# Optimization experiments

Measured on AMD Instinct MI355X. Metric: run time of the kernel, lower is better.

## Reference

```python
import jax, jax.numpy as jnp
import numpy as np

V, NB, NJ, NP, NK = 6890, 10, 24, 207, 19
PARENTS = np.array([-1, 0, 0, 0, 1, 2, 3, 4, 5, 6, 7, 8, 9, 9, 9, 12, 13, 14, 16, 17, 18, 19, 20, 21])


def setup_inputs():
    key = jax.random.key(0)
    ks = jax.random.split(key, 9)
    B = 1024
    beta = jax.random.normal(ks[0], (B, NB), jnp.float32)
    theta = jax.random.normal(ks[1], (B, NJ * 3), jnp.float32) * 0.3  # axis-angle per joint
    trans = jax.random.normal(ks[2], (B, 3), jnp.float32)
    v_template = jax.random.normal(ks[3], (V, 3), jnp.float32)
    shapedirs = jax.random.normal(ks[4], (NB, V * 3), jnp.float32) * 0.03
    Jr = jax.random.uniform(ks[5], (V, NJ), jnp.float32)
    J_regressor = Jr / jnp.sum(Jr, axis=0, keepdims=True)
    posedirs = jax.random.normal(ks[6], (NP, V * 3), jnp.float32) * 0.01
    jr = jax.random.uniform(ks[7], (V, NK), jnp.float32)
    joint_regressor = jr / jnp.sum(jr, axis=0, keepdims=True)
    w = jax.random.uniform(ks[8], (V, NJ), jnp.float32)
    weights = w / jnp.sum(w, axis=1, keepdims=True)  # LBS weights, rows sum to 1
    return dict(beta=beta, theta=theta, trans=trans, v_template=v_template,
                shapedirs=shapedirs, J_regressor=J_regressor, posedirs=posedirs,
                joint_regressor=joint_regressor, weights=weights)


def batch_rodrigues(theta):
    # theta: (N,3) axis-angle -> (N,3,3) rotation matrices via quaternions (HMR-style)
    angle = jnp.linalg.norm(theta + 1e-8, axis=1, keepdims=True)
    half = angle * 0.5
    v = (theta / angle) * jnp.sin(half)
    quat = jnp.concatenate([jnp.cos(half), v], axis=1)
    quat = quat / jnp.linalg.norm(quat, axis=1, keepdims=True)
    w, x, y, z = quat[:, 0], quat[:, 1], quat[:, 2], quat[:, 3]
    rot = jnp.stack([
        1 - 2 * (y * y + z * z), 2 * (x * y - w * z), 2 * (x * z + w * y),
        2 * (x * y + w * z), 1 - 2 * (x * x + z * z), 2 * (y * z - w * x),
        2 * (x * z - w * y), 2 * (y * z + w * x), 1 - 2 * (x * x + y * y)], axis=1)
    return rot.reshape(-1, 3, 3)


def batch_global_rigid_transformation(Rs, J):
    # Rs: (B,24,3,3), J: (B,24,3); rotate_base=True
    B = Rs.shape[0]
    rot_x = jnp.array([[1., 0., 0.], [0., -1., 0.], [0., 0., -1.]], jnp.float32)
    root_R = Rs[:, 0] @ rot_x

    def make_A(R, t):  # (B,3,3),(B,3) -> (B,4,4)
        top = jnp.concatenate([R, t[:, :, None]], axis=2)
        bot = jnp.broadcast_to(jnp.array([0., 0., 0., 1.], jnp.float32), (B, 1, 4))
        return jnp.concatenate([top, bot], axis=1)

    results = [make_A(root_R, J[:, 0])]
    for i in range(1, NJ):  # fixed 24-joint kinematic chain
        t = J[:, i] - J[:, PARENTS[i]]
        results.append(results[PARENTS[i]] @ make_A(Rs[:, i], t))
    res = jnp.stack(results, axis=1)  # (B,24,4,4)
    new_J = res[:, :, :3, 3]
    j_w0 = jnp.concatenate([J, jnp.zeros_like(J[:, :, :1])], axis=2)  # (B,24,4), homo w=0
    init_bone = jnp.einsum('bjrc,bjc->bjr', res, j_w0)
    A = res.at[:, :, :, 3].add(-init_bone)  # subtract only last column (matches F.pad trick)
    return new_J, A


def reference(beta, theta, trans, v_template, shapedirs, J_regressor, posedirs, joint_regressor, weights):
    B = beta.shape[0]
    v_shaped = (beta @ shapedirs).reshape(B, V, 3) + v_template
    J = jnp.einsum('bvc,vj->bjc', v_shaped, J_regressor)  # (B,24,3)
    Rs = batch_rodrigues(theta.reshape(-1, 3)).reshape(B, NJ, 3, 3)
    pose_feature = (Rs[:, 1:] - jnp.eye(3, dtype=Rs.dtype)).reshape(B, NP)
    v_posed = (pose_feature @ posedirs).reshape(B, V, 3) + v_shaped
    _, A = batch_global_rigid_transformation(Rs, J)
    T = jnp.einsum('vj,bjrc->bvrc', weights, A)  # (B,V,4,4) per-vertex skinning transforms
    homo = jnp.concatenate([v_posed, jnp.ones((B, V, 1), v_posed.dtype)], axis=2)
    verts = jnp.einsum('bvrc,bvc->bvr', T, homo)[:, :, :3] + trans[:, None, :]
    joints = jnp.einsum('bvc,vk->bkc', verts, joint_regressor)  # (B,19,3)
    return joints
```

## Files before the change

### kernel.cpp

```cpp
#include <hip/hip_runtime.h>
#include <hip/hip_bf16.h>

constexpr int Vn   = 6890;
constexpr int VC3  = 20670;
constexpr int NKB  = 216;
constexpr int QT   = 224;
constexpr int NMG  = 14;
constexpr int NCOL = 480;
constexpr int MC   = 1368;
constexpr int KCH  = 27;

using bf16x8  = __attribute__((ext_vector_type(8))) short;
using floatx4 = __attribute__((ext_vector_type(4))) float;

__device__ __forceinline__ unsigned short f2bf(float f) {
    unsigned int u = __float_as_uint(f);
    unsigned int r = (u + 0x7FFFu + ((u >> 16) & 1u)) >> 16;
    return (unsigned short)r;
}

__global__ __launch_bounds__(256) void k0_build(
    const float* __restrict__ vt, const float* __restrict__ sdirs,
    const float* __restrict__ pdirs, const float* __restrict__ Jreg,
    const float* __restrict__ jreg, const float* __restrict__ wts,
    unsigned short* __restrict__ Af, unsigned short* __restrict__ Bf)
{
    int bx = blockIdx.x, t = threadIdx.x;
    if (bx < 756) {
        int mg = bx / 54, ub = bx % 54;
        int ql = t & 15, q = mg * 16 + ql;
        int uu = ub * 16 + (t >> 4);
        int v0 = uu * 8, base = 3 * v0;
        float buf[24];
        if (q == 0) {
            #pragma unroll
            for (int i = 0; i < 24; ++i) buf[i] = (v0 + i / 3 < Vn) ? 1.f : 0.f;
        } else {
            const float* src = nullptr;
            if (q == 1) src = vt;
            else if (q >= 2 && q < 12)   src = sdirs + (size_t)(q - 2) * VC3;
            else if (q >= 12 && q < 219) src = pdirs + (size_t)(q - 12) * VC3;
            if (src && base + 23 < VC3) {
                #pragma unroll
                for (int i = 0; i < 12; ++i) {
                    float2 f = *(const float2*)(src + base + 2 * i);
                    buf[2 * i] = f.x; buf[2 * i + 1] = f.y;
                }
            } else {
                #pragma unroll
                for (int i = 0; i < 24; ++i)
                    buf[i] = (src && base + i < VC3) ? src[base + i] : 0.f;
            }
        }
        int kb = uu >> 2, quad = uu & 3;
        size_t foff = (size_t)(ql + quad * 16) * 8;
        #pragma unroll
        for (int c = 0; c < 3; ++c) {
            bf16x8 o;
            #pragma unroll
            for (int j = 0; j < 8; ++j) o[j] = (short)f2bf(buf[3 * j + c]);
            *(bf16x8*)(Af + ((size_t)(c * NMG + mg) * NKB + kb) * 512 + foff) = o;
        }
        return;
    }
    bx -= 756;
    {
        int v0 = bx * 64;
        __shared__ float js[64 * 19], wsh[64 * 24], Jsh[64 * 24];
        for (int i = t; i < 64 * 19; i += 256)
            js[i] = (v0 * 19 + i < Vn * 19) ? jreg[v0 * 19 + i] : 0.f;
        for (int i = t; i < 64 * 24; i += 256) {
            wsh[i] = (v0 * 24 + i < Vn * 24) ? wts[v0 * 24 + i] : 0.f;
            Jsh[i] = (v0 * 24 + i < Vn * 24) ? Jreg[v0 * 24 + i] : 0.f;
        }
        __syncthreads();
        for (int s = t; s < 4096; s += 256) {
            int clow = s & 15, w = s >> 4;
            int vg = w & 7, chigh = w >> 3;
            int col = chigh * 16 + clow;
            int kb = (v0 >> 5) + (vg >> 2);
            bf16x8 o;
            #pragma unroll
            for (int j = 0; j < 8; ++j) {
                int vl = vg * 8 + j;
                float val = 0.f;
                if (col < 456)      val = js[vl * 19 + col / 24] * wsh[vl * 24 + col % 24];
                else if (col < 480) val = Jsh[vl * 24 + (col - 456)];
                o[j] = (short)f2bf(val);
            }
            *(bf16x8*)(Bf + ((size_t)chigh * NKB + kb) * 512
                          + (size_t)(clow + (vg & 3) * 16) * 8) = o;
        }
    }
}

__device__ __forceinline__ void k1_load(bf16x8 (&a)[2], bf16x8 (&b)[4],
    const unsigned short* __restrict__ ap, const unsigned short* __restrict__ bp, int i)
{
    a[0] = *(const bf16x8*)(ap + (size_t)(0 * NKB + i) * 512);
    a[1] = *(const bf16x8*)(ap + (size_t)(1 * NKB + i) * 512);
    b[0] = *(const bf16x8*)(bp + (size_t)(0 * NKB + i) * 512);
    b[1] = *(const bf16x8*)(bp + (size_t)(1 * NKB + i) * 512);
    b[2] = *(const bf16x8*)(bp + (size_t)(2 * NKB + i) * 512);
    b[3] = *(const bf16x8*)(bp + (size_t)(3 * NKB + i) * 512);
}

__global__ __launch_bounds__(512) void k1_mfma(
    const unsigned short* __restrict__ Af, const unsigned short* __restrict__ Bf,
    unsigned short* __restrict__ Wb3, float* __restrict__ w1g,
    float* __restrict__ Jacc)
{
    __shared__ float red[8 * 2048];
    int tid = threadIdx.x;
    int wv = tid >> 6, l = tid & 63;
    int r = blockIdx.x;
    int c = r / 56; r %= 56;
    int mt = r >> 3, nt = r & 7;
    int kb0 = wv * KCH;

    const unsigned short* ap = Af + ((size_t)(c * NMG + mt * 2) * NKB + kb0) * 512 + l * 8;
    const unsigned short* bp = Bf + ((size_t)(nt * 4) * NKB + kb0) * 512 + l * 8;

    floatx4 acc[2][4];
    #pragma unroll
    for (int mi = 0; mi < 2; ++mi)
        #pragma unroll
        for (int ni = 0; ni < 4; ++ni) acc[mi][ni] = floatx4{0.f, 0.f, 0.f, 0.f};

    bf16x8 a[3][2], b[3][4];
    k1_load(a[0], b[0], ap, bp, 0);
    k1_load(a[1], b[1], ap, bp, 1);
    #pragma unroll
    for (int i = 0; i < KCH; ++i) {
        if (i + 2 < KCH) k1_load(a[(i + 2) % 3], b[(i + 2) % 3], ap, bp, i + 2);
        bf16x8 (&ac)[2] = a[i % 3];
        bf16x8 (&bc)[4] = b[i % 3];
        #pragma unroll
        for (int mi = 0; mi < 2; ++mi)
            #pragma unroll
            for (int ni = 0; ni < 4; ++ni)
                acc[mi][ni] = __builtin_amdgcn_mfma_f32_16x16x32_bf16(ac[mi], bc[ni], acc[mi][ni], 0, 0, 0);
    }
    #pragma unroll
    for (int mi = 0; mi < 2; ++mi)
        #pragma unroll
        for (int ni = 0; ni < 4; ++ni)
            *(floatx4*)&red[wv * 2048 + ((mi * 4 + ni) * 64 + l) * 4] = acc[mi][ni];
    __syncthreads();
    if (tid < 256) {
        int cl = tid & 63, qo = tid >> 6;
        int ni = cl >> 4;
        int q0 = qo * 8;
        int li0 = ((q0 & 15) >> 2) * 16 + (cl & 15);
        int li1 = (((q0 + 4) & 15) >> 2) * 16 + (cl & 15);
        int base0 = (((q0 >> 4) * 4 + ni) * 64 + li0) * 4;
        int base1 = ((((q0 + 4) >> 4) * 4 + ni) * 64 + li1) * 4;
        floatx4 s0{0.f, 0.f, 0.f, 0.f}, s1{0.f, 0.f, 0.f, 0.f};
        #pragma unroll
        for (int ww = 0; ww < 8; ++ww) {
            s0 += *(const floatx4*)&red[ww * 2048 + base0];
            s1 += *(const floatx4*)&red[ww * 2048 + base1];
        }
        int col = nt * 64 + cl;
        if (col < NCOL) {
            int colc = col * 3 + c;
            if (colc < MC) {
                bf16x8 o;
                #pragma unroll
                for (int j = 0; j < 4; ++j) {
                    o[j]     = (short)f2bf(s0[j]);
                    o[4 + j] = (short)f2bf(s1[j]);
                }
                *(bf16x8*)(Wb3 + ((size_t)(colc >> 4) * 7 + mt) * 512
                               + (size_t)((colc & 15) + qo * 16) * 8) = o;
            }
            if (c == 0 && mt == 0 && qo == 0 && col < 456) w1g[col] = s0[0];
            if (mt == 0 && col >= 456) {
                float* jb = Jacc + (size_t)((col - 456) * 3 + c) * 11;
                if (qo == 0) {
                    jb[0] = s0[1]; jb[1] = s0[2]; jb[2] = s0[3];
                    jb[3] = s1[0]; jb[4] = s1[1]; jb[5] = s1[2]; jb[6] = s1[3];
                } else if (qo == 1) {
                    jb[7] = s0[0]; jb[8] = s0[1]; jb[9] = s0[2]; jb[10] = s0[3];
                }
            }
        }
    }
}

__global__ __launch_bounds__(512) void k2_tail(
    const unsigned short* __restrict__ Wb3, const float* __restrict__ Jacc,
    const float* __restrict__ w1g, const float* __restrict__ beta,
    const float* __restrict__ theta, const float* __restrict__ trans,
    float* __restrict__ out)
{
    __shared__ float Rs[16][24][9];
    __shared__ float Jl[16][24][3];
    __shared__ float resR[16][24][9];
    __shared__ float rest_[16][24][3];
    __shared__ float tAs[16][72];
    __shared__ float bet[16][10];
    __shared__ float Jas[792];
    __shared__ float w1s[456];
    __shared__ unsigned short xls[7 * 512];
    __shared__ float Msh[16][145];
    int t = threadIdx.x;
    int bt = blockIdx.x / 10, kp = blockIdx.x % 10;
    int b0 = bt * 16;
    int nmg = (kp == 9) ? 5 : 9;
    int mgbase = kp * 9;

    if (t < 160) bet[t / 10][t % 10] = beta[(b0 + t / 10) * 10 + t % 10];
    for (int i = t; i < 792; i += 512) Jas[i] = Jacc[i];
    if (t < 456) w1s[t] = w1g[t];
    if (t >= 128 && t < 512) {
        int i = t - 128;
        int bl = i / 24, j = i % 24;
        float t0 = theta[(size_t)(b0 + bl) * 72 + j * 3 + 0];
        float t1 = theta[(size_t)(b0 + bl) * 72 + j * 3 + 1];
        float t2 = theta[(size_t)(b0 + bl) * 72 + j * 3 + 2];
        float e0 = t0 + 1e-8f, e1 = t1 + 1e-8f, e2 = t2 + 1e-8f;
        float angle = sqrtf(e0 * e0 + e1 * e1 + e2 * e2);
        float half = 0.5f * angle;
        float sh = sinf(half), ch = cosf(half);
        float s = sh / angle;
        float qx = t0 * s, qy = t1 * s, qz = t2 * s;
        float qn = sqrtf(ch * ch + qx * qx + qy * qy + qz * qz);
        float w = ch / qn, x = qx / qn, y = qy / qn, z = qz / qn;
        Rs[bl][j][0] = 1.f - 2.f * (y * y + z * z);
        Rs[bl][j][1] = 2.f * (x * y - w * z);
        Rs[bl][j][2] = 2.f * (x * z + w * y);
        Rs[bl][j][3] = 2.f * (x * y + w * z);
        Rs[bl][j][4] = 1.f - 2.f * (x * x + z * z);
        Rs[bl][j][5] = 2.f * (y * z - w * x);
        Rs[bl][j][6] = 2.f * (x * z - w * y);
        Rs[bl][j][7] = 2.f * (y * z + w * x);
        Rs[bl][j][8] = 1.f - 2.f * (x * x + y * y);
    }
    __syncthreads();
    for (int i = t; i < 16 * 72; i += 512) {
        int bl = i / 72, jc = i % 72;
        const float* bp_ = Jas + (size_t)jc * 11;
        float a = bp_[0];
        #pragma unroll
        for (int n = 0; n < 10; ++n) a += bet[bl][n] * bp_[1 + n];
        Jl[bl][jc / 3][jc % 3] = a;
    }
    __syncthreads();
    for (int i = t; i < 16 * QT; i += 512) {
        int q = i >> 4, bl = i & 15;
        float xv = 0.f;
        if (q == 1) xv = 1.f;
        else if (q >= 2 && q < 12) xv = bet[bl][q - 2];
        else if (q >= 12 && q < 219) {
            int p = q - 12;
            int jj = 1 + p / 9, e = p % 9;
            float rr = Rs[bl][jj][e];
            if (e == 0 || e == 4 || e == 8) rr -= 1.f;
            xv = rr;
        }
        xls[(size_t)(q >> 5) * 512 + (size_t)(bl + ((q >> 3) & 3) * 16) * 8 + (q & 7)]
            = f2bf(xv);
    }
    __syncthreads();
    int wv = t >> 6, l = t & 63;
    if (wv == 0) {
        if (t < 48) {
            const int par[24] = {-1,0,0,0,1,2,3,4,5,6,7,8,9,9,9,12,13,14,16,17,18,19,20,21};
            int bl = t / 3, rr = t % 3;
            resR[bl][0][rr * 3 + 0] =  Rs[bl][0][rr * 3 + 0];
            resR[bl][0][rr * 3 + 1] = -Rs[bl][0][rr * 3 + 1];
            resR[bl][0][rr * 3 + 2] = -Rs[bl][0][rr * 3 + 2];
            rest_[bl][0][rr] = Jl[bl][0][rr];
            for (int i = 1; i < 24; ++i) {
                int p = par[i];
                float t0 = Jl[bl][i][0] - Jl[bl][p][0];
                float t1 = Jl[bl][i][1] - Jl[bl][p][1];
                float t2 = Jl[bl][i][2] - Jl[bl][p][2];
                float a0 = resR[bl][p][rr * 3 + 0], a1 = resR[bl][p][rr * 3 + 1],
                      a2 = resR[bl][p][rr * 3 + 2];
                resR[bl][i][rr * 3 + 0] = a0 * Rs[bl][i][0] + a1 * Rs[bl][i][3] + a2 * Rs[bl][i][6];
                resR[bl][i][rr * 3 + 1] = a0 * Rs[bl][i][1] + a1 * Rs[bl][i][4] + a2 * Rs[bl][i][7];
                resR[bl][i][rr * 3 + 2] = a0 * Rs[bl][i][2] + a1 * Rs[bl][i][5] + a2 * Rs[bl][i][8];
                rest_[bl][i][rr] = a0 * t0 + a1 * t1 + a2 * t2 + rest_[bl][p][rr];
            }
        }
    } else {
        for (int mgl = wv - 1; mgl < nmg; mgl += 7) {
            const unsigned short* ap = Wb3 + (size_t)(mgbase + mgl) * 7 * 512 + l * 8;
            floatx4 acc{0.f, 0.f, 0.f, 0.f};
            #pragma unroll
            for (int kk = 0; kk < 7; ++kk)
                acc = __builtin_amdgcn_mfma_f32_16x16x32_bf16(
                    *(const bf16x8*)(ap + (size_t)kk * 512),
                    *(const bf16x8*)(xls + (size_t)kk * 512 + l * 8), acc, 0, 0, 0);
            int bl = l & 15, cc0 = mgl * 16 + (l >> 4) * 4;
            #pragma unroll
            for (int rr = 0; rr < 4; ++rr) Msh[bl][cc0 + rr] = acc[rr];
        }
    }
    __syncthreads();
    for (int i = t; i < 16 * 72; i += 512) {
        int bl = i / 72, jc = i % 72;
        int j = jc / 3, c = jc % 3;
        tAs[bl][jc] = rest_[bl][j][c]
            - (resR[bl][j][c * 3 + 0] * Jl[bl][j][0] + resR[bl][j][c * 3 + 1] * Jl[bl][j][1]
             + resR[bl][j][c * 3 + 2] * Jl[bl][j][2]);
    }
    __syncthreads();
    int nk = (kp == 9) ? 1 : 2;
    for (int i = t; i < 48 * nk; i += 512) {
        int kl = i / 48, r2 = i % 48;
        int bl = r2 / 3, c = r2 % 3;
        int b = b0 + bl, k = kp * 2 + kl;
        float s = trans[b * 3 + c];
        const float* mrow = Msh[bl] + kl * 72;
        #pragma unroll
        for (int j = 0; j < 24; ++j) {
            s += tAs[bl][j * 3 + c] * w1s[k * 24 + j];
            s += resR[bl][j][c * 3 + 0] * mrow[j * 3 + 0]
               + resR[bl][j][c * 3 + 1] * mrow[j * 3 + 1]
               + resR[bl][j][c * 3 + 2] * mrow[j * 3 + 2];
        }
        out[(size_t)b * 57 + k * 3 + c] = s;
    }
}

extern "C" void kernel_launch(void* const* d_in, const int* in_sizes, int n_in,
                              void* d_out, int out_size, void* d_ws, size_t ws_size,
                              hipStream_t stream)
{
    const float* beta  = (const float*)d_in[0];
    const float* theta = (const float*)d_in[1];
    const float* trans = (const float*)d_in[2];
    const float* vt    = (const float*)d_in[3];
    const float* sdirs = (const float*)d_in[4];
    const float* Jreg  = (const float*)d_in[5];
    const float* pdirs = (const float*)d_in[6];
    const float* jreg  = (const float*)d_in[7];
    const float* wts   = (const float*)d_in[8];
    float* out = (float*)d_out;
    int B = in_sizes[0] / 10;

    unsigned short* Af  = (unsigned short*)d_ws;
    unsigned short* Bf  = Af + (size_t)42 * NKB * 512;
    unsigned short* Wb3 = Bf + (size_t)32 * NKB * 512;
    float* Jacc = (float*)(Wb3 + (size_t)88 * 7 * 512);
    float* w1g  = Jacc + 792;

    k0_build<<<dim3(756 + 108), 256, 0, stream>>>(
        vt, sdirs, pdirs, Jreg, jreg, wts, Af, Bf);
    k1_mfma<<<dim3(168), 512, 0, stream>>>(Af, Bf, Wb3, w1g, Jacc);
    k2_tail<<<dim3((B / 16) * 10), 512, 0, stream>>>(
        Wb3, Jacc, w1g, beta, theta, trans, out);
}
```

Baseline: 130.3 us.

## Precompute per-batch rotations and bf16 pose features in build kernel

Moves the Rodrigues rotation computation and the bf16 packing of the pose/shape feature vector out of the tail kernel, where each of the 10 k-partition blocks per batch tile recomputed them, into extra blocks of the first kernel that write them once to workspace. The tail kernel then loads rotations from global memory and feeds the MFMA B operand straight from global. It also drops the shared Jacc copy and the tAs staging pass by recomputing the translation term inline in the final reduction. This cuts redundant transcendental work and two barriers, at the cost of extra global traffic and more redundant arithmetic in the output loop.

```diff
diff --git a/kernel.cpp b/kernel.cpp
--- a/kernel.cpp
+++ b/kernel.cpp
@@ -23,8 +23,11 @@
     const float* __restrict__ vt, const float* __restrict__ sdirs,
     const float* __restrict__ pdirs, const float* __restrict__ Jreg,
     const float* __restrict__ jreg, const float* __restrict__ wts,
-    unsigned short* __restrict__ Af, unsigned short* __restrict__ Bf)
-{
+    const float* __restrict__ beta, const float* __restrict__ theta,
+    unsigned short* __restrict__ Af, unsigned short* __restrict__ Bf,
+    float* __restrict__ Rsg, unsigned short* __restrict__ xbf)
+{
+    __shared__ float Rc[16][24][9];
     int bx = blockIdx.x, t = threadIdx.x;
     if (bx < 756) {
         int mg = bx / 54, ub = bx % 54;
@@ -64,7 +67,7 @@
         return;
     }
     bx -= 756;
-    {
+    if (bx < 108) {
         int v0 = bx * 64;
         __shared__ float js[64 * 19], wsh[64 * 24], Jsh[64 * 24];
         for (int i = t; i < 64 * 19; i += 256)
@@ -90,6 +93,58 @@
             }
             *(bf16x8*)(Bf + ((size_t)chigh * NKB + kb) * 512
                           + (size_t)(clow + (vg & 3) * 16) * 8) = o;
+        }
+        return;
+    }
+    bx -= 108;
+    {
+        int b0 = bx * 16;
+        for (int i = t; i < 384; i += 256) {
+            int bl = i / 24, j = i % 24;
+            float t0 = theta[(size_t)(b0 + bl) * 72 + j * 3 + 0];
+            float t1 = theta[(size_t)(b0 + bl) * 72 + j * 3 + 1];
+            float t2 = theta[(size_t)(b0 + bl) * 72 + j * 3 + 2];
+            float e0 = t0 + 1e-8f, e1 = t1 + 1e-8f, e2 = t2 + 1e-8f;
+            float angle = sqrtf(e0 * e0 + e1 * e1 + e2 * e2);
+            float half = 0.5f * angle;
+            float sh = sinf(half), ch = cosf(half);
+            float s = sh / angle;
+            float qx = t0 * s, qy = t1 * s, qz = t2 * s;
+            float qn = sqrtf(ch * ch + qx * qx + qy * qy + qz * qz);
+            float w = ch / qn, x = qx / qn, y = qy / qn, z = qz / qn;
+            float r0 = 1.f - 2.f * (y * y + z * z);
+            float r1 = 2.f * (x * y - w * z);
+            float r2 = 2.f * (x * z + w * y);
+            float r3 = 2.f * (x * y + w * z);
+            float r4 = 1.f - 2.f * (x * x + z * z);
+            float r5 = 2.f * (y * z - w * x);
+            float r6 = 2.f * (x * z - w * y);
+            float r7 = 2.f * (y * z + w * x);
+            float r8 = 1.f - 2.f * (x * x + y * y);
+            Rc[bl][j][0] = r0; Rc[bl][j][1] = r1; Rc[bl][j][2] = r2;
+            Rc[bl][j][3] = r3; Rc[bl][j][4] = r4; Rc[bl][j][5] = r5;
+            Rc[bl][j][6] = r6; Rc[bl][j][7] = r7; Rc[bl][j][8] = r8;
+            float* rg = Rsg + (size_t)(b0 + bl) * 216 + j * 9;
+            rg[0] = r0; rg[1] = r1; rg[2] = r2;
+            rg[3] = r3; rg[4] = r4; rg[5] = r5;
+            rg[6] = r6; rg[7] = r7; rg[8] = r8;
+        }
+        __syncthreads();
+        for (int i = t; i < 16 * QT; i += 256) {
+            int q = i >> 4, bl = i & 15;
+            int b = b0 + bl;
+            float xv = 0.f;
+            if (q == 1) xv = 1.f;
+            else if (q >= 2 && q < 12) xv = beta[(size_t)b * 10 + (q - 2)];
+            else if (q >= 12 && q < 219) {
+                int p = q - 12;
+                int jj = 1 + p / 9, e = p % 9;
+                float rr = Rc[bl][jj][e];
+                if (e == 0 || e == 4 || e == 8) rr -= 1.f;
+                xv = rr;
+            }
+            xbf[((size_t)(b >> 4) * 7 + (q >> 5)) * 512
+                + (size_t)((b & 15) + ((q >> 3) & 3) * 16) * 8 + (q & 7)] = f2bf(xv);
         }
     }
 }
@@ -189,20 +244,17 @@
 }
 
 __global__ __launch_bounds__(512) void k2_tail(
-    const unsigned short* __restrict__ Wb3, const float* __restrict__ Jacc,
+    const unsigned short* __restrict__ Wb3, const unsigned short* __restrict__ xbf,
+    const float* __restrict__ Rsg, const float* __restrict__ Jacc,
     const float* __restrict__ w1g, const float* __restrict__ beta,
-    const float* __restrict__ theta, const float* __restrict__ trans,
-    float* __restrict__ out)
+    const float* __restrict__ trans, float* __restrict__ out)
 {
     __shared__ float Rs[16][24][9];
     __shared__ float Jl[16][24][3];
     __shared__ float resR[16][24][9];
     __shared__ float rest_[16][24][3];
-    __shared__ float tAs[16][72];
     __shared__ float bet[16][10];
-    __shared__ float Jas[792];
     __shared__ float w1s[456];
-    __shared__ unsigned short xls[7 * 512];
     __shared__ float Msh[16][145];
     int t = threadIdx.x;
     int bt = blockIdx.x / 10, kp = blockIdx.x % 10;
@@ -211,56 +263,17 @@
     int mgbase = kp * 9;
 
     if (t < 160) bet[t / 10][t % 10] = beta[(b0 + t / 10) * 10 + t % 10];
-    for (int i = t; i < 792; i += 512) Jas[i] = Jacc[i];
     if (t < 456) w1s[t] = w1g[t];
-    if (t >= 128 && t < 512) {
-        int i = t - 128;
-        int bl = i / 24, j = i % 24;
-        float t0 = theta[(size_t)(b0 + bl) * 72 + j * 3 + 0];
-        float t1 = theta[(size_t)(b0 + bl) * 72 + j * 3 + 1];
-        float t2 = theta[(size_t)(b0 + bl) * 72 + j * 3 + 2];
-        float e0 = t0 + 1e-8f, e1 = t1 + 1e-8f, e2 = t2 + 1e-8f;
-        float angle = sqrtf(e0 * e0 + e1 * e1 + e2 * e2);
-        float half = 0.5f * angle;
-        float sh = sinf(half), ch = cosf(half);
-        float s = sh / angle;
-        float qx = t0 * s, qy = t1 * s, qz = t2 * s;
-        float qn = sqrtf(ch * ch + qx * qx + qy * qy + qz * qz);
-        float w = ch / qn, x = qx / qn, y = qy / qn, z = qz / qn;
-        Rs[bl][j][0] = 1.f - 2.f * (y * y + z * z);
-        Rs[bl][j][1] = 2.f * (x * y - w * z);
-        Rs[bl][j][2] = 2.f * (x * z + w * y);
-        Rs[bl][j][3] = 2.f * (x * y + w * z);
-        Rs[bl][j][4] = 1.f - 2.f * (x * x + z * z);
-        Rs[bl][j][5] = 2.f * (y * z - w * x);
-        Rs[bl][j][6] = 2.f * (x * z - w * y);
-        Rs[bl][j][7] = 2.f * (y * z + w * x);
-        Rs[bl][j][8] = 1.f - 2.f * (x * x + y * y);
-    }
+    for (int i = t; i < 3456; i += 512)
+        ((float*)Rs)[i] = Rsg[(size_t)b0 * 216 + i];
     __syncthreads();
     for (int i = t; i < 16 * 72; i += 512) {
         int bl = i / 72, jc = i % 72;
-        const float* bp_ = Jas + (size_t)jc * 11;
+        const float* bp_ = Jacc + (size_t)jc * 11;
         float a = bp_[0];
         #pragma unroll
         for (int n = 0; n < 10; ++n) a += bet[bl][n] * bp_[1 + n];
         Jl[bl][jc / 3][jc % 3] = a;
-    }
-    __syncthreads();
-    for (int i = t; i < 16 * QT; i += 512) {
-        int q = i >> 4, bl = i & 15;
-        float xv = 0.f;
-        if (q == 1) xv = 1.f;
-        else if (q >= 2 && q < 12) xv = bet[bl][q - 2];
-        else if (q >= 12 && q < 219) {
-            int p = q - 12;
-            int jj = 1 + p / 9, e = p % 9;
-            float rr = Rs[bl][jj][e];
-            if (e == 0 || e == 4 || e == 8) rr -= 1.f;
-            xv = rr;
-        }
-        xls[(size_t)(q >> 5) * 512 + (size_t)(bl + ((q >> 3) & 3) * 16) * 8 + (q & 7)]
-            = f2bf(xv);
     }
     __syncthreads();
     int wv = t >> 6, l = t & 63;
@@ -286,6 +299,7 @@
             }
         }
     } else {
+        const unsigned short* bp = xbf + (size_t)bt * 7 * 512 + l * 8;
         for (int mgl = wv - 1; mgl < nmg; mgl += 7) {
             const unsigned short* ap = Wb3 + (size_t)(mgbase + mgl) * 7 * 512 + l * 8;
             floatx4 acc{0.f, 0.f, 0.f, 0.f};
@@ -293,19 +307,11 @@
             for (int kk = 0; kk < 7; ++kk)
                 acc = __builtin_amdgcn_mfma_f32_16x16x32_bf16(
                     *(const bf16x8*)(ap + (size_t)kk * 512),
-                    *(const bf16x8*)(xls + (size_t)kk * 512 + l * 8), acc, 0, 0, 0);
+                    *(const bf16x8*)(bp + (size_t)kk * 512), acc, 0, 0, 0);
             int bl = l & 15, cc0 = mgl * 16 + (l >> 4) * 4;
             #pragma unroll
             for (int rr = 0; rr < 4; ++rr) Msh[bl][cc0 + rr] = acc[rr];
         }
-    }
-    __syncthreads();
-    for (int i = t; i < 16 * 72; i += 512) {
-        int bl = i / 72, jc = i % 72;
-        int j = jc / 3, c = jc % 3;
-        tAs[bl][jc] = rest_[bl][j][c]
-            - (resR[bl][j][c * 3 + 0] * Jl[bl][j][0] + resR[bl][j][c * 3 + 1] * Jl[bl][j][1]
-             + resR[bl][j][c * 3 + 2] * Jl[bl][j][2]);
     }
     __syncthreads();
     int nk = (kp == 9) ? 1 : 2;
@@ -317,7 +323,11 @@
         const float* mrow = Msh[bl] + kl * 72;
         #pragma unroll
         for (int j = 0; j < 24; ++j) {
-            s += tAs[bl][j * 3 + c] * w1s[k * 24 + j];
+            float ta = rest_[bl][j][c]
+                - (resR[bl][j][c * 3 + 0] * Jl[bl][j][0]
+                 + resR[bl][j][c * 3 + 1] * Jl[bl][j][1]
+                 + resR[bl][j][c * 3 + 2] * Jl[bl][j][2]);
+            s += ta * w1s[k * 24 + j];
             s += resR[bl][j][c * 3 + 0] * mrow[j * 3 + 0]
                + resR[bl][j][c * 3 + 1] * mrow[j * 3 + 1]
                + resR[bl][j][c * 3 + 2] * mrow[j * 3 + 2];
@@ -345,12 +355,14 @@
     unsigned short* Af  = (unsigned short*)d_ws;
     unsigned short* Bf  = Af + (size_t)42 * NKB * 512;
     unsigned short* Wb3 = Bf + (size_t)32 * NKB * 512;
-    float* Jacc = (float*)(Wb3 + (size_t)88 * 7 * 512);
+    unsigned short* xbf = Wb3 + (size_t)88 * 7 * 512;
+    float* Jacc = (float*)(xbf + (size_t)64 * 7 * 512);
     float* w1g  = Jacc + 792;
-
-    k0_build<<<dim3(756 + 108), 256, 0, stream>>>(
-        vt, sdirs, pdirs, Jreg, jreg, wts, Af, Bf);
+    float* Rsg  = w1g + 456;
+
+    k0_build<<<dim3(756 + 108 + 64), 256, 0, stream>>>(
+        vt, sdirs, pdirs, Jreg, jreg, wts, beta, theta, Af, Bf, Rsg, xbf);
     k1_mfma<<<dim3(168), 512, 0, stream>>>(Af, Bf, Wb3, w1g, Jacc);
     k2_tail<<<dim3((B / 16) * 10), 512, 0, stream>>>(
-        Wb3, Jacc, w1g, beta, theta, trans, out);
-}
+        Wb3, xbf, Rsg, Jacc, w1g, beta, trans, out);
+}
```

Result: faster. 126.9 us (-2.6%).
